# Performance work log

Measured on AMD Instinct MI355X. Metric: run time of the kernel, lower is better.

## Reference

```python
import jax, jax.numpy as jnp
import numpy as np

B, L, D, H, DEPTH = 64, 384, 128, 8, 6
DH = D // H          # 16
VOCAB = 32000
C_OUT = 128
FF = 4 * D           # reformer_pytorch default ff_mult=4
SELF_VAL = -5e4      # TOKEN_SELF_ATTN_VALUE
MASK_VAL = -1e9      # causal mask value


def layer_norm(x, g, b, eps=1e-5):
    mu = jnp.mean(x, -1, keepdims=True)
    var = jnp.mean((x - mu) ** 2, -1, keepdims=True)
    return (x - mu) * jax.lax.rsqrt(var + eps) * g + b


def attn_block(x, p):
    # PreNorm + LSHSelfAttention in full-QK-attention fallback (seq <= full_attn_thres)
    h = layer_norm(x, p['ln1_g'], p['ln1_b'])
    qk = (h @ p['Wqk']).reshape(B, L, H, DH).transpose(0, 2, 1, 3)  # [B,H,L,DH]
    v = (h @ p['Wv']).reshape(B, L, H, DH).transpose(0, 2, 1, 3)
    # shared QK: q = qk, k = l2-normalized qk
    k = qk / jnp.maximum(jnp.linalg.norm(qk, axis=-1, keepdims=True), 1e-12)
    dots = jnp.einsum('bhid,bhjd->bhij', qk, k) * (DH ** -0.5)
    i = jnp.arange(L)
    eye = i[:, None] == i[None, :]
    future = i[None, :] > i[:, None]
    dots = jnp.where(eye, SELF_VAL, dots)   # token cannot (easily) attend to itself
    dots = jnp.where(future, MASK_VAL, dots)  # causal
    a = jax.nn.softmax(dots, axis=-1)
    o = jnp.einsum('bhij,bhjd->bhid', a, v).transpose(0, 2, 1, 3).reshape(B, L, D)
    return o @ p['Wo'] + p['bo']


def ff_block(x, p):
    h = layer_norm(x, p['ln2_g'], p['ln2_b'])
    h = jax.nn.gelu(h @ p['W1'] + p['b1'], approximate=False)
    return h @ p['W2'] + p['b2']


def forward(x_enc, emb, pos1, pos2, ln1_g, ln1_b, Wqk, Wv, Wo, bo,
            ln2_g, ln2_b, W1, b1, W2, b2, lnf_g, lnf_b, Wp, bp):
    # axial positional embedding (summed mode): (25,D) + (25,D) -> (625,D)
    pos = (pos1[:, None, :] + pos2[None, :, :]).reshape(25 * 25, D)[:L]
    x = emb[x_enc] + pos  # [B,L,D]

    layer_params = dict(ln1_g=ln1_g, ln1_b=ln1_b, Wqk=Wqk, Wv=Wv, Wo=Wo, bo=bo,
                        ln2_g=ln2_g, ln2_b=ln2_b, W1=W1, b1=b1, W2=W2, b2=b2)

    def block(carry, p):
        x1, x2 = carry
        y1 = x1 + attn_block(x2, p)
        y2 = x2 + ff_block(y1, p)
        return (y1, y2), None

    # reversible-net math: duplicate stream, run blocks, average the two halves
    (x1, x2), _ = jax.lax.scan(block, (x, x), layer_params)
    x = layer_norm((x1 + x2) * 0.5, lnf_g, lnf_b)
    return x.reshape(B, L * D) @ Wp + bp  # [B, C_OUT]


def setup_inputs() -> dict:
    key = jax.random.key(0)
    ks = jax.random.split(key, 12)
    s = 0.02
    inp = {
        'x_enc': jax.random.randint(ks[0], (B, L), 0, VOCAB, dtype=jnp.int32),
        'emb': jax.random.normal(ks[1], (VOCAB, D), jnp.float32) * s,
        'pos1': jax.random.normal(ks[2], (25, D), jnp.float32) * s,
        'pos2': jax.random.normal(ks[3], (25, D), jnp.float32) * s,
        'ln1_g': jnp.ones((DEPTH, D), jnp.float32),
        'ln1_b': jnp.zeros((DEPTH, D), jnp.float32),
        'Wqk': jax.random.normal(ks[4], (DEPTH, D, D), jnp.float32) * s,
        'Wv': jax.random.normal(ks[5], (DEPTH, D, D), jnp.float32) * s,
        'Wo': jax.random.normal(ks[6], (DEPTH, D, D), jnp.float32) * s,
        'bo': jnp.zeros((DEPTH, D), jnp.float32),
        'ln2_g': jnp.ones((DEPTH, D), jnp.float32),
        'ln2_b': jnp.zeros((DEPTH, D), jnp.float32),
        'W1': jax.random.normal(ks[7], (DEPTH, D, FF), jnp.float32) * s,
        'b1': jnp.zeros((DEPTH, FF), jnp.float32),
        'W2': jax.random.normal(ks[8], (DEPTH, FF, D), jnp.float32) * s,
        'b2': jnp.zeros((DEPTH, D), jnp.float32),
        'lnf_g': jnp.ones((D,), jnp.float32),
        'lnf_b': jnp.zeros((D,), jnp.float32),
        'Wp': jax.random.normal(ks[9], (L * D, C_OUT), jnp.float32) * s,
        'bp': jnp.zeros((C_OUT,), jnp.float32),
    }
    return inp


def reference(x_enc, emb, pos1, pos2, ln1_g, ln1_b, Wqk, Wv, Wo, bo,
              ln2_g, ln2_b, W1, b1, W2, b2, lnf_g, lnf_b, Wp, bp):
    return forward(x_enc, emb, pos1, pos2, ln1_g, ln1_b, Wqk, Wv, Wo, bo,
                   ln2_g, ln2_b, W1, b1, W2, b2, lnf_g, lnf_b, Wp, bp)
```

## Files before the change

### kernel.cpp

```cpp
#include <hip/hip_runtime.h>
#include <hip/hip_bf16.h>
#include <math.h>

#define BB 64
#define LL 384
#define DD 128
#define HH 8
#define DHH 16
#define DEPTH 6
#define FFD 512
#define MROWS (BB*LL)
#define COUT 128
#define KP (LL*DD)
#define KSPLIT 96
#define KCHUNK 512

typedef short bf16x8 __attribute__((ext_vector_type(8)));
typedef float f32x4 __attribute__((ext_vector_type(4)));

__device__ __forceinline__ unsigned short f2bs(float x) {
    __hip_bfloat16 h = __float2bfloat16(x);
    return *reinterpret_cast<unsigned short*>(&h);
}
__device__ __forceinline__ float bs2f(unsigned short u) {
    unsigned int v = ((unsigned int)u) << 16;
    return __uint_as_float(v);
}

__global__ __launch_bounds__(256) void embed_kernel(
    const int* __restrict__ x_enc, const float* __restrict__ emb,
    const float* __restrict__ pos1, const float* __restrict__ pos2,
    float* __restrict__ x1, float* __restrict__ x2)
{
    int t = blockIdx.x * 256 + threadIdx.x;
    int row = t >> 5;
    int c4 = t & 31;
    int l = row % LL;
    int tok = x_enc[row];
    float4 a = ((const float4*)(emb + (size_t)tok * DD))[c4];
    float4 b = ((const float4*)(pos1 + (l / 25) * DD))[c4];
    float4 c = ((const float4*)(pos2 + (l % 25) * DD))[c4];
    float4 r = make_float4(a.x + b.x + c.x, a.y + b.y + c.y,
                           a.z + b.z + c.z, a.w + b.w + c.w);
    ((float4*)x1)[t] = r;
    ((float4*)x2)[t] = r;
}

__global__ __launch_bounds__(256) void castT_kernel(
    const float* __restrict__ src, __hip_bfloat16* __restrict__ dst, int K, int N,
    long sstride, long dstride)
{
    __shared__ float tile[32][33];
    int kb = blockIdx.x * 32, nb = blockIdx.y * 32;
    int tx = threadIdx.x & 31, ty = threadIdx.x >> 5;
    const float* s = src + (size_t)blockIdx.z * sstride;
    __hip_bfloat16* d = dst + (size_t)blockIdx.z * dstride;
    #pragma unroll
    for (int r = 0; r < 32; r += 8)
        tile[r + ty][tx] = s[(size_t)(kb + r + ty) * N + nb + tx];
    __syncthreads();
    #pragma unroll
    for (int r = 0; r < 32; r += 8)
        d[(size_t)(nb + r + ty) * K + kb + tx] = __float2bfloat16(tile[tx][r + ty]);
}

__global__ __launch_bounds__(256) void castT3_kernel(
    const float* __restrict__ sqk, const float* __restrict__ sv, const float* __restrict__ so,
    __hip_bfloat16* __restrict__ dqk, __hip_bfloat16* __restrict__ dv,
    __hip_bfloat16* __restrict__ dwo)
{
    __shared__ float tile[32][33];
    int which = blockIdx.z / 6;
    int dd = blockIdx.z % 6;
    const float* s = (which == 0 ? sqk : (which == 1 ? sv : so)) + (size_t)dd * 16384;
    __hip_bfloat16* d = (which == 0 ? dqk : (which == 1 ? dv : dwo))
                        + (size_t)dd * (which == 2 ? 16384 : 32768);
    int kb = blockIdx.x * 32, nb = blockIdx.y * 32;
    int tx = threadIdx.x & 31, ty = threadIdx.x >> 5;
    #pragma unroll
    for (int r = 0; r < 32; r += 8)
        tile[r + ty][tx] = s[(size_t)(kb + r + ty) * 128 + nb + tx];
    __syncthreads();
    #pragma unroll
    for (int r = 0; r < 32; r += 8)
        d[(size_t)(nb + r + ty) * 128 + kb + tx] = __float2bfloat16(tile[tx][r + ty]);
}

__global__ __launch_bounds__(256) void ln_kernel(
    const float* __restrict__ x, const float* __restrict__ g,
    const float* __restrict__ b, __hip_bfloat16* __restrict__ y)
{
    int wave = threadIdx.x >> 6;
    int lane = threadIdx.x & 63;
    int row = blockIdx.x * 4 + wave;
    float2 v = ((const float2*)(x + (size_t)row * DD))[lane];
    float2 gg = ((const float2*)g)[lane];
    float2 bb = ((const float2*)b)[lane];
    float s = v.x + v.y;
    float sq = v.x * v.x + v.y * v.y;
    #pragma unroll
    for (int off = 32; off > 0; off >>= 1) {
        s += __shfl_down(s, off, 64);
        sq += __shfl_down(sq, off, 64);
    }
    s = __shfl(s, 0, 64);
    sq = __shfl(sq, 0, 64);
    float mean = s * (1.0f / DD);
    float var = sq * (1.0f / DD) - mean * mean;
    float rstd = rsqrtf(var + 1e-5f);
    __hip_bfloat16* yp = y + (size_t)row * DD + lane * 2;
    yp[0] = __float2bfloat16((v.x - mean) * rstd * gg.x + bb.x);
    yp[1] = __float2bfloat16((v.y - mean) * rstd * gg.y + bb.y);
}

__device__ __forceinline__ float gelu_exact(float x) {
    return 0.5f * x * (1.0f + erff(x * 0.70710678118654752f));
}

template<int K, int N, bool BIAS, bool RES, bool GELU, bool OBF, bool LNOUT, bool AVGLN>
__global__ __launch_bounds__(256) void gemm_bf16(
    const __hip_bfloat16* __restrict__ A, const __hip_bfloat16* __restrict__ Bt,
    const float* __restrict__ bias, const float* __restrict__ Rsrc,
    const float* __restrict__ Rsrc2,
    void* __restrict__ Cdst,
    const float* __restrict__ lng, const float* __restrict__ lnb,
    __hip_bfloat16* __restrict__ lnout)
{
    __shared__ unsigned short As[64 * 128];
    __shared__ unsigned short Bs[128 * 128];
    int tid = threadIdx.x;
    int l = tid & 63, w = tid >> 6;
    int wr = w >> 1, wc = w & 1;
    int lr = l & 15, q = l >> 4;
    int m0 = blockIdx.y * 64;
    int n0 = blockIdx.x * 128;

    f32x4 acc[2][4];
    #pragma unroll
    for (int mt = 0; mt < 2; ++mt)
        #pragma unroll
        for (int nt = 0; nt < 4; ++nt) acc[mt][nt] = (f32x4){0.f, 0.f, 0.f, 0.f};

    for (int kt = 0; kt < K; kt += 128) {
        if (kt) __syncthreads();
        #pragma unroll
        for (int p = 0; p < 4; ++p) {
            int n = p * 256 + tid;
            int r = n >> 4;
            int c = (n & 15) ^ (r & 7);
            uint4 dv = *(const uint4*)(A + (size_t)(m0 + r) * K + kt + c * 8);
            *(uint4*)&As[n * 8] = dv;
        }
        #pragma unroll
        for (int p = 0; p < 8; ++p) {
            int n = p * 256 + tid;
            int r = n >> 4;
            int c = (n & 15) ^ (r & 7);
            uint4 dv = *(const uint4*)(Bt + (size_t)(n0 + r) * K + kt + c * 8);
            *(uint4*)&Bs[n * 8] = dv;
        }
        __syncthreads();

        #pragma unroll
        for (int kk = 0; kk < 4; ++kk) {
            bf16x8 afr[2], bfr[4];
            #pragma unroll
            for (int mt = 0; mt < 2; ++mt) {
                int rA = wr * 32 + mt * 16 + lr;
                int cc = (kk * 4 + q) ^ (rA & 7);
                afr[mt] = *(const bf16x8*)&As[(rA * 16 + cc) * 8];
            }
            #pragma unroll
            for (int nt = 0; nt < 4; ++nt) {
                int rB = wc * 64 + nt * 16 + lr;
                int cc = (kk * 4 + q) ^ (rB & 7);
                bfr[nt] = *(const bf16x8*)&Bs[(rB * 16 + cc) * 8];
            }
            #pragma unroll
            for (int mt = 0; mt < 2; ++mt)
                #pragma unroll
                for (int nt = 0; nt < 4; ++nt)
                    acc[mt][nt] = __builtin_amdgcn_mfma_f32_16x16x32_bf16(
                        afr[mt], bfr[nt], acc[mt][nt], 0, 0, 0);
        }
    }

    if (!LNOUT) {
        #pragma unroll
        for (int mt = 0; mt < 2; ++mt) {
            #pragma unroll
            for (int nt = 0; nt < 4; ++nt) {
                int col = n0 + wc * 64 + nt * 16 + lr;
                float bv = BIAS ? bias[col] : 0.f;
                #pragma unroll
                for (int r = 0; r < 4; ++r) {
                    int row = m0 + wr * 32 + mt * 16 + q * 4 + r;
                    float val = acc[mt][nt][r] + bv;
                    if (GELU) val = gelu_exact(val);
                    if (RES) val += Rsrc[(size_t)row * N + col];
                    if (OBF) ((__hip_bfloat16*)Cdst)[(size_t)row * N + col] = __float2bfloat16(val);
                    else     ((float*)Cdst)[(size_t)row * N + col] = val;
                }
            }
        }
    } else {
        float* fp = (float*)Bs;
        __syncthreads();
        #pragma unroll
        for (int mt = 0; mt < 2; ++mt) {
            #pragma unroll
            for (int nt = 0; nt < 4; ++nt) {
                int col = wc * 64 + nt * 16 + lr;
                float bv = BIAS ? bias[col] : 0.f;
                #pragma unroll
                for (int r = 0; r < 4; ++r) {
                    int rowL = wr * 32 + mt * 16 + q * 4 + r;
                    float val = acc[mt][nt][r] + bv;
                    if (RES) val += Rsrc[(size_t)(m0 + rowL) * N + col];
                    fp[rowL * 128 + col] = val;
                }
            }
        }
        __syncthreads();
        int rl = tid >> 2, sub = tid & 3;
        float s = 0.f, sq = 0.f;
        #pragma unroll
        for (int c4 = 0; c4 < 8; ++c4) {
            float4 v = *(const float4*)&fp[rl * 128 + sub * 32 + c4 * 4];
            if (AVGLN) {
                float4 xo = *(const float4*)(Rsrc2 + (size_t)(m0 + rl) * 128 + sub * 32 + c4 * 4);
                v.x = (v.x + xo.x) * 0.5f; v.y = (v.y + xo.y) * 0.5f;
                v.z = (v.z + xo.z) * 0.5f; v.w = (v.w + xo.w) * 0.5f;
            }
            s  += (v.x + v.y) + (v.z + v.w);
            sq += (v.x * v.x + v.y * v.y) + (v.z * v.z + v.w * v.w);
        }
        s  += __shfl_xor(s, 1);  s  += __shfl_xor(s, 2);
        sq += __shfl_xor(sq, 1); sq += __shfl_xor(sq, 2);
        float mean = s * (1.0f / 128.0f);
        float var  = sq * (1.0f / 128.0f) - mean * mean;
        float rstd = rsqrtf(var + 1e-5f);
        int rowG = m0 + rl;
        #pragma unroll
        for (int c4 = 0; c4 < 8; ++c4) {
            int col = sub * 32 + c4 * 4;
            float4 v  = *(const float4*)&fp[rl * 128 + col];
            if (AVGLN) {
                float4 xo = *(const float4*)(Rsrc2 + (size_t)rowG * 128 + col);
                v.x = (v.x + xo.x) * 0.5f; v.y = (v.y + xo.y) * 0.5f;
                v.z = (v.z + xo.z) * 0.5f; v.w = (v.w + xo.w) * 0.5f;
            } else {
                *(float4*)((float*)Cdst + (size_t)rowG * 128 + col) = v;
            }
            float4 g4 = *(const float4*)(lng + col);
            float4 b4 = *(const float4*)(lnb + col);
            unsigned short pk[4];
            pk[0] = f2bs((v.x - mean) * rstd * g4.x + b4.x);
            pk[1] = f2bs((v.y - mean) * rstd * g4.y + b4.y);
            pk[2] = f2bs((v.z - mean) * rstd * g4.z + b4.z);
            pk[3] = f2bs((v.w - mean) * rstd * g4.w + b4.w);
            *(ushort4*)((unsigned short*)lnout + (size_t)rowG * 128 + col) = *(ushort4*)&pk[0];
        }
    }
}

__global__ __launch_bounds__(256) void attn_kernel(
    const __hip_bfloat16* __restrict__ qkv, __hip_bfloat16* __restrict__ o)
{
    int z  = blockIdx.x >> 9;
    int bh = blockIdx.x & 511;
    int b = bh >> 3, hh = bh & 7;
    const unsigned short* base = (const unsigned short*)qkv + (size_t)b * LL * 256 + hh * DHH;

    __shared__ unsigned short knb[LL + 2][24];
    __shared__ unsigned short vtb[16][LL + 24];
    __shared__ float cq[LL];
    __shared__ unsigned short ptile[4][16][40];

    int t = threadIdx.x;
    for (int r = t; r < LL; r += 256) {
        const unsigned short* qp = base + (size_t)r * 256;
        unsigned short qs[16], vs16[16];
        *(uint4*)&qs[0]  = *(const uint4*)(qp);
        *(uint4*)&qs[8]  = *(const uint4*)(qp + 8);
        *(uint4*)&vs16[0] = *(const uint4*)(qp + 128);
        *(uint4*)&vs16[8] = *(const uint4*)(qp + 136);
        float q[16];
        #pragma unroll
        for (int d = 0; d < 16; ++d) q[d] = bs2f(qs[d]);
        float nrm = 0.f;
        #pragma unroll
        for (int d = 0; d < 16; ++d) nrm = fmaf(q[d], q[d], nrm);
        float qn = sqrtf(nrm);
        float inv = 1.0f / fmaxf(qn, 1e-12f);
        cq[r] = 0.25f * qn;
        unsigned short kb[16];
        #pragma unroll
        for (int d = 0; d < 16; ++d) kb[d] = f2bs(q[d] * inv);
        *(uint4*)&knb[r][0] = *(uint4*)&kb[0];
        *(uint4*)&knb[r][8] = *(uint4*)&kb[8];
        *(uint4*)&knb[r][16] = make_uint4(0u, 0u, 0u, 0u);
        #pragma unroll
        for (int d = 0; d < 16; ++d) vtb[d][r] = vs16[d];
    }
    if (t < 16) {
        #pragma unroll
        for (int c = 0; c < 24; ++c) vtb[t][LL + c] = 0;
    }
    if (t < 2) {
        #pragma unroll
        for (int c = 0; c < 24; ++c) knb[LL + t][c] = 0;
    }

    int w = t >> 6, l = t & 63;
    int lr = l & 15, q4 = l >> 4;
    __syncthreads();

    bf16x8 zfrag = {0, 0, 0, 0, 0, 0, 0, 0};
    bf16x8 onesf;
    #pragma unroll
    for (int i = 0; i < 8; ++i) onesf[i] = (short)0x3F80;

    int slot = 2 * w + z;
    int strips[3] = { slot, 15 - slot, 16 + slot };
    #pragma unroll
    for (int si = 0; si < 3; ++si) {
        int s = strips[si];
        int r0 = s * 16;
        bf16x8 bq = *(const bf16x8*)&knb[r0 + lr][q4 * 8];
        float ccq = cq[r0 + lr];
        int qg = r0 + lr;

        f32x4 oacc = (f32x4){0.f, 0.f, 0.f, 0.f};
        f32x4 lacc = (f32x4){0.f, 0.f, 0.f, 0.f};

        for (int jt = 0; jt <= s; jt += 2) {
            bf16x8 a0 = *(const bf16x8*)&knb[jt * 16 + lr][(q4 & 1) * 8];
            a0 = (q4 < 2) ? a0 : zfrag;
            bf16x8 a1 = *(const bf16x8*)&knb[(jt + 1) * 16 + lr][(q4 & 1) * 8];
            a1 = (q4 < 2) ? a1 : zfrag;
            f32x4 s0 = __builtin_amdgcn_mfma_f32_16x16x32_bf16(
                a0, bq, (f32x4){0.f, 0.f, 0.f, 0.f}, 0, 0, 0);
            f32x4 s1 = __builtin_amdgcn_mfma_f32_16x16x32_bf16(
                a1, bq, (f32x4){0.f, 0.f, 0.f, 0.f}, 0, 0, 0);

            unsigned int pk0[2], pk1[2];
            #pragma unroll
            for (int h = 0; h < 2; ++h) {
                int ja = jt * 16 + q4 * 4 + 2 * h;
                float pa = __expf(fmaf(s0[2 * h],     ccq, -ccq));
                pa = (ja < qg) ? pa : 0.f;
                float pb = __expf(fmaf(s0[2 * h + 1], ccq, -ccq));
                pb = (ja + 1 < qg) ? pb : 0.f;
                pk0[h] = (unsigned int)f2bs(pa) | ((unsigned int)f2bs(pb) << 16);
                float pc = __expf(fmaf(s1[2 * h],     ccq, -ccq));
                pc = (ja + 16 < qg) ? pc : 0.f;
                float pd = __expf(fmaf(s1[2 * h + 1], ccq, -ccq));
                pd = (ja + 17 < qg) ? pd : 0.f;
                pk1[h] = (unsigned int)f2bs(pc) | ((unsigned int)f2bs(pd) << 16);
            }
            *(uint2*)&ptile[w][lr][q4 * 4]      = make_uint2(pk0[0], pk0[1]);
            *(uint2*)&ptile[w][lr][16 + q4 * 4] = make_uint2(pk1[0], pk1[1]);
            asm volatile("s_waitcnt lgkmcnt(0)" ::: "memory");
            bf16x8 pfrag = *(const bf16x8*)&ptile[w][lr][q4 * 8];
            bf16x8 vfrag = *(const bf16x8*)&vtb[lr][jt * 16 + q4 * 8];
            oacc = __builtin_amdgcn_mfma_f32_16x16x32_bf16(pfrag, vfrag, oacc, 0, 0, 0);
            lacc = __builtin_amdgcn_mfma_f32_16x16x32_bf16(pfrag, onesf, lacc, 0, 0, 0);
        }

        if (s == 0 && q4 == 0) {
            lacc[0] = 1.0f;
            oacc[0] = bs2f(vtb[lr][0]);
        }
        unsigned short* ob = (unsigned short*)o + (size_t)(b * LL + r0) * DD + hh * 16 + lr;
        #pragma unroll
        for (int reg = 0; reg < 4; ++reg) {
            float ov = oacc[reg] / lacc[reg];
            ob[(size_t)(q4 * 4 + reg) * DD] = f2bs(ov);
        }
    }
}

__global__ __launch_bounds__(256) void final_mfma_kernel(
    const __hip_bfloat16* __restrict__ A, const __hip_bfloat16* __restrict__ Bt,
    float* __restrict__ partials)
{
    __shared__ unsigned short As[64 * 128];
    __shared__ unsigned short Bs[128 * 128];
    int tid = threadIdx.x;
    int l = tid & 63, w = tid >> 6;
    int wr = w >> 1, wc = w & 1;
    int lr = l & 15, q = l >> 4;
    int kbase = blockIdx.x * KCHUNK;

    f32x4 acc[2][4];
    #pragma unroll
    for (int mt = 0; mt < 2; ++mt)
        #pragma unroll
        for (int nt = 0; nt < 4; ++nt) acc[mt][nt] = (f32x4){0.f, 0.f, 0.f, 0.f};

    for (int kt = 0; kt < KCHUNK; kt += 128) {
        if (kt) __syncthreads();
        #pragma unroll
        for (int p = 0; p < 4; ++p) {
            int n = p * 256 + tid;
            int r = n >> 4;
            int c = (n & 15) ^ (r & 7);
            uint4 dv = *(const uint4*)(A + (size_t)r * KP + kbase + kt + c * 8);
            *(uint4*)&As[n * 8] = dv;
        }
        #pragma unroll
        for (int p = 0; p < 8; ++p) {
            int n = p * 256 + tid;
            int r = n >> 4;
            int c = (n & 15) ^ (r & 7);
            uint4 dv = *(const uint4*)(Bt + (size_t)r * KP + kbase + kt + c * 8);
            *(uint4*)&Bs[n * 8] = dv;
        }
        __syncthreads();

        #pragma unroll
        for (int kk = 0; kk < 4; ++kk) {
            bf16x8 afr[2], bfr[4];
            #pragma unroll
            for (int mt = 0; mt < 2; ++mt) {
                int rA = wr * 32 + mt * 16 + lr;
                int cc = (kk * 4 + q) ^ (rA & 7);
                afr[mt] = *(const bf16x8*)&As[(rA * 16 + cc) * 8];
            }
            #pragma unroll
            for (int nt = 0; nt < 4; ++nt) {
                int rB = wc * 64 + nt * 16 + lr;
                int cc = (kk * 4 + q) ^ (rB & 7);
                bfr[nt] = *(const bf16x8*)&Bs[(rB * 16 + cc) * 8];
            }
            #pragma unroll
            for (int mt = 0; mt < 2; ++mt)
                #pragma unroll
                for (int nt = 0; nt < 4; ++nt)
                    acc[mt][nt] = __builtin_amdgcn_mfma_f32_16x16x32_bf16(
                        afr[mt], bfr[nt], acc[mt][nt], 0, 0, 0);
        }
    }

    float* dst = partials + (size_t)blockIdx.x * (64 * 128);
    #pragma unroll
    for (int mt = 0; mt < 2; ++mt) {
        #pragma unroll
        for (int nt = 0; nt < 4; ++nt) {
            int col = wc * 64 + nt * 16 + lr;
            #pragma unroll
            for (int r = 0; r < 4; ++r) {
                int row = wr * 32 + mt * 16 + q * 4 + r;
                dst[row * 128 + col] = acc[mt][nt][r];
            }
        }
    }
}

__global__ __launch_bounds__(256) void final_reduce_kernel(
    const float* __restrict__ partials, const float* __restrict__ bp,
    float* __restrict__ out)
{
    int j = blockIdx.x * 256 + threadIdx.x;
    float s = bp[j & (COUT - 1)];
    #pragma unroll 8
    for (int p = 0; p < KSPLIT; ++p)
        s += partials[(size_t)p * 8192 + j];
    out[j] = s;
}

extern "C" void kernel_launch(void* const* d_in, const int* in_sizes, int n_in,
                              void* d_out, int out_size, void* d_ws, size_t ws_size,
                              hipStream_t stream)
{
    const int*   x_enc = (const int*)  d_in[0];
    const float* emb   = (const float*)d_in[1];
    const float* pos1  = (const float*)d_in[2];
    const float* pos2  = (const float*)d_in[3];
    const float* ln1_g = (const float*)d_in[4];
    const float* ln1_b = (const float*)d_in[5];
    const float* Wqk   = (const float*)d_in[6];
    const float* Wv    = (const float*)d_in[7];
    const float* Wo    = (const float*)d_in[8];
    const float* bo    = (const float*)d_in[9];
    const float* ln2_g = (const float*)d_in[10];
    const float* ln2_b = (const float*)d_in[11];
    const float* W1    = (const float*)d_in[12];
    const float* b1    = (const float*)d_in[13];
    const float* W2    = (const float*)d_in[14];
    const float* b2    = (const float*)d_in[15];
    const float* lnf_g = (const float*)d_in[16];
    const float* lnf_b = (const float*)d_in[17];
    const float* Wp    = (const float*)d_in[18];
    const float* bp    = (const float*)d_in[19];
    float* out = (float*)d_out;

    const size_t SZ = (size_t)MROWS * DD;
    float* ws_f = (float*)d_ws;
    float* x1 = ws_f;
    float* x2 = ws_f + SZ;
    float* R  = ws_f + 2 * SZ;
    __hip_bfloat16* qkv_bf = (__hip_bfloat16*)R;
    __hip_bfloat16* hff = (__hip_bfloat16*)R;
    __hip_bfloat16* h_bf = (__hip_bfloat16*)(ws_f + 4 * SZ);
    __hip_bfloat16* o_bf = h_bf + SZ;
    __hip_bfloat16* wqvT = o_bf + SZ;
    __hip_bfloat16* woT  = wqvT + 6 * 32768;
    __hip_bfloat16* w1T  = woT  + 6 * 16384;
    __hip_bfloat16* w2T  = w1T  + 6 * 65536;
    __hip_bfloat16* WpT  = w2T  + 6 * 65536;
    float* partials = (float*)(WpT + (size_t)COUT * KP);

    castT3_kernel<<<dim3(4, 4, 18), dim3(256), 0, stream>>>(
        Wqk, Wv, Wo, wqvT, wqvT + 16384, woT);
    castT_kernel<<<dim3(4, 16, 6), dim3(256), 0, stream>>>(W1, w1T, 128, 512, 65536, 65536);
    castT_kernel<<<dim3(16, 4, 6), dim3(256), 0, stream>>>(W2, w2T, 512, 128, 65536, 65536);
    castT_kernel<<<dim3(KP / 32, 4, 1), dim3(256), 0, stream>>>(Wp, WpT, KP, 128, 0, 0);

    embed_kernel<<<dim3(MROWS * 32 / 256), dim3(256), 0, stream>>>(x_enc, emb, pos1, pos2, x1, x2);
    ln_kernel<<<dim3(MROWS / 4), dim3(256), 0, stream>>>(x2, ln1_g, ln1_b, h_bf);

    for (int d = 0; d < DEPTH; ++d) {
        const float* bod = bo + d * DD;
        const float* l2g = ln2_g + d * DD;
        const float* l2b = ln2_b + d * DD;
        const float* b1d = b1 + d * FFD;
        const float* b2d = b2 + d * DD;
        const __hip_bfloat16* wqv_d = wqvT + (size_t)d * 32768;
        const __hip_bfloat16* wo_d  = woT  + (size_t)d * 16384;
        const __hip_bfloat16* w1_d  = w1T  + (size_t)d * 65536;
        const __hip_bfloat16* w2_d  = w2T  + (size_t)d * 65536;

        gemm_bf16<128, 256, false, false, false, true, false, false>
            <<<dim3(2, MROWS / 64), dim3(256), 0, stream>>>(
                h_bf, wqv_d, nullptr, nullptr, nullptr, qkv_bf, nullptr, nullptr, nullptr);
        attn_kernel<<<dim3(BB * HH * 2), dim3(256), 0, stream>>>(qkv_bf, o_bf);
        gemm_bf16<128, 128, true, true, false, false, true, false>
            <<<dim3(1, MROWS / 64), dim3(256), 0, stream>>>(
                o_bf, wo_d, bod, x1, nullptr, x1, l2g, l2b, h_bf);
        gemm_bf16<128, 512, true, false, true, true, false, false>
            <<<dim3(4, MROWS / 64), dim3(256), 0, stream>>>(
                h_bf, w1_d, b1d, nullptr, nullptr, hff, nullptr, nullptr, nullptr);
        if (d < DEPTH - 1) {
            gemm_bf16<512, 128, true, true, false, false, true, false>
                <<<dim3(1, MROWS / 64), dim3(256), 0, stream>>>(
                    hff, w2_d, b2d, x2, nullptr, x2,
                    ln1_g + (d + 1) * DD, ln1_b + (d + 1) * DD, h_bf);
        } else {
            gemm_bf16<512, 128, true, true, false, false, true, true>
                <<<dim3(1, MROWS / 64), dim3(256), 0, stream>>>(
                    hff, w2_d, b2d, x2, x1, nullptr, lnf_g, lnf_b, h_bf);
        }
    }

    final_mfma_kernel<<<dim3(KSPLIT), dim3(256), 0, stream>>>(h_bf, WpT, partials);
    final_reduce_kernel<<<dim3(32), dim3(256), 0, stream>>>(partials, bp, out);
}
```

Before: 674.5 us.

## Fuse Wo+LN2+W1 and W2+LN1+QKV GEMMs into per-row-tile mega kernels

Merges the Wo projection, residual, LayerNorm and W1+GELU GEMM into one kernel that keeps the normalized tile in shared memory. It likewise merges the W2 GEMM, residual, next-layer LN1 and the next layer's QKV projection. The goal is to remove round trips through global memory for h_bf and to cut per-layer launches. It also fuses embedding with the first LayerNorm, merges the weight-cast launches, and reuses the WpT buffer as QKV scratch, casting Wp only at the end. In exchange, each block now runs several GEMM stages serially with more shared memory, which may lower occupancy.

Result: faster. 619.2 us (-8.2%).

```diff
diff --git a/kernel.cpp b/kernel.cpp
--- a/kernel.cpp
+++ b/kernel.cpp
@@ -26,74 +26,28 @@
     unsigned int v = ((unsigned int)u) << 16;
     return __uint_as_float(v);
 }
-
-__global__ __launch_bounds__(256) void embed_kernel(
+__device__ __forceinline__ float gelu_exact(float x) {
+    return 0.5f * x * (1.0f + erff(x * 0.70710678118654752f));
+}
+
+__global__ __launch_bounds__(256) void embedln_kernel(
     const int* __restrict__ x_enc, const float* __restrict__ emb,
     const float* __restrict__ pos1, const float* __restrict__ pos2,
-    float* __restrict__ x1, float* __restrict__ x2)
-{
-    int t = blockIdx.x * 256 + threadIdx.x;
-    int row = t >> 5;
-    int c4 = t & 31;
-    int l = row % LL;
-    int tok = x_enc[row];
-    float4 a = ((const float4*)(emb + (size_t)tok * DD))[c4];
-    float4 b = ((const float4*)(pos1 + (l / 25) * DD))[c4];
-    float4 c = ((const float4*)(pos2 + (l % 25) * DD))[c4];
-    float4 r = make_float4(a.x + b.x + c.x, a.y + b.y + c.y,
-                           a.z + b.z + c.z, a.w + b.w + c.w);
-    ((float4*)x1)[t] = r;
-    ((float4*)x2)[t] = r;
-}
-
-__global__ __launch_bounds__(256) void castT_kernel(
-    const float* __restrict__ src, __hip_bfloat16* __restrict__ dst, int K, int N,
-    long sstride, long dstride)
-{
-    __shared__ float tile[32][33];
-    int kb = blockIdx.x * 32, nb = blockIdx.y * 32;
-    int tx = threadIdx.x & 31, ty = threadIdx.x >> 5;
-    const float* s = src + (size_t)blockIdx.z * sstride;
-    __hip_bfloat16* d = dst + (size_t)blockIdx.z * dstride;
-    #pragma unroll
-    for (int r = 0; r < 32; r += 8)
-        tile[r + ty][tx] = s[(size_t)(kb + r + ty) * N + nb + tx];
-    __syncthreads();
-    #pragma unroll
-    for (int r = 0; r < 32; r += 8)
-        d[(size_t)(nb + r + ty) * K + kb + tx] = __float2bfloat16(tile[tx][r + ty]);
-}
-
-__global__ __launch_bounds__(256) void castT3_kernel(
-    const float* __restrict__ sqk, const float* __restrict__ sv, const float* __restrict__ so,
-    __hip_bfloat16* __restrict__ dqk, __hip_bfloat16* __restrict__ dv,
-    __hip_bfloat16* __restrict__ dwo)
-{
-    __shared__ float tile[32][33];
-    int which = blockIdx.z / 6;
-    int dd = blockIdx.z % 6;
-    const float* s = (which == 0 ? sqk : (which == 1 ? sv : so)) + (size_t)dd * 16384;
-    __hip_bfloat16* d = (which == 0 ? dqk : (which == 1 ? dv : dwo))
-                        + (size_t)dd * (which == 2 ? 16384 : 32768);
-    int kb = blockIdx.x * 32, nb = blockIdx.y * 32;
-    int tx = threadIdx.x & 31, ty = threadIdx.x >> 5;
-    #pragma unroll
-    for (int r = 0; r < 32; r += 8)
-        tile[r + ty][tx] = s[(size_t)(kb + r + ty) * 128 + nb + tx];
-    __syncthreads();
-    #pragma unroll
-    for (int r = 0; r < 32; r += 8)
-        d[(size_t)(nb + r + ty) * 128 + kb + tx] = __float2bfloat16(tile[tx][r + ty]);
-}
-
-__global__ __launch_bounds__(256) void ln_kernel(
-    const float* __restrict__ x, const float* __restrict__ g,
-    const float* __restrict__ b, __hip_bfloat16* __restrict__ y)
+    const float* __restrict__ g, const float* __restrict__ b,
+    float* __restrict__ x1, float* __restrict__ x2,
+    __hip_bfloat16* __restrict__ y)
 {
     int wave = threadIdx.x >> 6;
     int lane = threadIdx.x & 63;
     int row = blockIdx.x * 4 + wave;
-    float2 v = ((const float2*)(x + (size_t)row * DD))[lane];
+    int l = row % LL;
+    int tok = x_enc[row];
+    float2 e  = ((const float2*)(emb + (size_t)tok * DD))[lane];
+    float2 p1 = ((const float2*)(pos1 + (l / 25) * DD))[lane];
+    float2 p2 = ((const float2*)(pos2 + (l % 25) * DD))[lane];
+    float2 v = make_float2(e.x + p1.x + p2.x, e.y + p1.y + p2.y);
+    ((float2*)(x1 + (size_t)row * DD))[lane] = v;
+    ((float2*)(x2 + (size_t)row * DD))[lane] = v;
     float2 gg = ((const float2*)g)[lane];
     float2 bb = ((const float2*)b)[lane];
     float s = v.x + v.y;
@@ -113,18 +67,58 @@
     yp[1] = __float2bfloat16((v.y - mean) * rstd * gg.y + bb.y);
 }
 
-__device__ __forceinline__ float gelu_exact(float x) {
-    return 0.5f * x * (1.0f + erff(x * 0.70710678118654752f));
-}
-
-template<int K, int N, bool BIAS, bool RES, bool GELU, bool OBF, bool LNOUT, bool AVGLN>
-__global__ __launch_bounds__(256) void gemm_bf16(
+__device__ __forceinline__ void castT_body(
+    const float* __restrict__ s, __hip_bfloat16* __restrict__ d,
+    int K, int N, int kb, int nb)
+{
+    __shared__ float tile[32][33];
+    int tx = threadIdx.x & 31, ty = threadIdx.x >> 5;
+    #pragma unroll
+    for (int r = 0; r < 32; r += 8)
+        tile[r + ty][tx] = s[(size_t)(kb + r + ty) * N + nb + tx];
+    __syncthreads();
+    #pragma unroll
+    for (int r = 0; r < 32; r += 8)
+        d[(size_t)(nb + r + ty) * K + kb + tx] = __float2bfloat16(tile[tx][r + ty]);
+}
+
+__global__ __launch_bounds__(256) void cast_all_kernel(
+    const float* __restrict__ Wqk, const float* __restrict__ Wv,
+    const float* __restrict__ Wo,  const float* __restrict__ W1,
+    const float* __restrict__ W2,
+    __hip_bfloat16* __restrict__ dqk, __hip_bfloat16* __restrict__ dv,
+    __hip_bfloat16* __restrict__ dwo, __hip_bfloat16* __restrict__ d1,
+    __hip_bfloat16* __restrict__ d2)
+{
+    int z = blockIdx.x;
+    if (z < 288) {
+        int m = z >> 4, t = z & 15;
+        int which = m / 6, dd = m % 6;
+        const float* s = (which == 0 ? Wqk : (which == 1 ? Wv : Wo)) + (size_t)dd * 16384;
+        __hip_bfloat16* d = (which == 0 ? dqk : (which == 1 ? dv : dwo))
+                            + (size_t)dd * (which == 2 ? 16384 : 32768);
+        castT_body(s, d, 128, 128, (t >> 2) * 32, (t & 3) * 32);
+    } else if (z < 672) {
+        int i = z - 288; int dd = i >> 6; int t = i & 63;
+        castT_body(W1 + (size_t)dd * 65536, d1 + (size_t)dd * 65536,
+                   128, 512, (t >> 4) * 32, (t & 15) * 32);
+    } else {
+        int i = z - 672; int dd = i >> 6; int t = i & 63;
+        castT_body(W2 + (size_t)dd * 65536, d2 + (size_t)dd * 65536,
+                   512, 128, (t >> 2) * 32, (t & 3) * 32);
+    }
+}
+
+__global__ __launch_bounds__(256) void castWp_kernel(
+    const float* __restrict__ src, __hip_bfloat16* __restrict__ dst)
+{
+    castT_body(src, dst, KP, 128, blockIdx.x * 32, blockIdx.y * 32);
+}
+
+template<int K, int N>
+__global__ __launch_bounds__(256) void gemm_qkv_kernel(
     const __hip_bfloat16* __restrict__ A, const __hip_bfloat16* __restrict__ Bt,
-    const float* __restrict__ bias, const float* __restrict__ Rsrc,
-    const float* __restrict__ Rsrc2,
-    void* __restrict__ Cdst,
-    const float* __restrict__ lng, const float* __restrict__ lnb,
-    __hip_bfloat16* __restrict__ lnout)
+    __hip_bfloat16* __restrict__ Cdst)
 {
     __shared__ unsigned short As[64 * 128];
     __shared__ unsigned short Bs[128 * 128];
@@ -148,19 +142,16 @@
             int n = p * 256 + tid;
             int r = n >> 4;
             int c = (n & 15) ^ (r & 7);
-            uint4 dv = *(const uint4*)(A + (size_t)(m0 + r) * K + kt + c * 8);
-            *(uint4*)&As[n * 8] = dv;
+            *(uint4*)&As[n * 8] = *(const uint4*)(A + (size_t)(m0 + r) * K + kt + c * 8);
         }
         #pragma unroll
         for (int p = 0; p < 8; ++p) {
             int n = p * 256 + tid;
             int r = n >> 4;
             int c = (n & 15) ^ (r & 7);
-            uint4 dv = *(const uint4*)(Bt + (size_t)(n0 + r) * K + kt + c * 8);
-            *(uint4*)&Bs[n * 8] = dv;
+            *(uint4*)&Bs[n * 8] = *(const uint4*)(Bt + (size_t)(n0 + r) * K + kt + c * 8);
         }
         __syncthreads();
-
         #pragma unroll
         for (int kk = 0; kk < 4; ++kk) {
             bf16x8 afr[2], bfr[4];
@@ -185,83 +176,17 @@
         }
     }
 
-    if (!LNOUT) {
-        #pragma unroll
-        for (int mt = 0; mt < 2; ++mt) {
-            #pragma unroll
-            for (int nt = 0; nt < 4; ++nt) {
-                int col = n0 + wc * 64 + nt * 16 + lr;
-                float bv = BIAS ? bias[col] : 0.f;
-                #pragma unroll
-                for (int r = 0; r < 4; ++r) {
-                    int row = m0 + wr * 32 + mt * 16 + q * 4 + r;
-                    float val = acc[mt][nt][r] + bv;
-                    if (GELU) val = gelu_exact(val);
-                    if (RES) val += Rsrc[(size_t)row * N + col];
-                    if (OBF) ((__hip_bfloat16*)Cdst)[(size_t)row * N + col] = __float2bfloat16(val);
-                    else     ((float*)Cdst)[(size_t)row * N + col] = val;
-                }
-            }
-        }
-    } else {
-        float* fp = (float*)Bs;
-        __syncthreads();
-        #pragma unroll
-        for (int mt = 0; mt < 2; ++mt) {
-            #pragma unroll
-            for (int nt = 0; nt < 4; ++nt) {
-                int col = wc * 64 + nt * 16 + lr;
-                float bv = BIAS ? bias[col] : 0.f;
-                #pragma unroll
-                for (int r = 0; r < 4; ++r) {
-                    int rowL = wr * 32 + mt * 16 + q * 4 + r;
-                    float val = acc[mt][nt][r] + bv;
-                    if (RES) val += Rsrc[(size_t)(m0 + rowL) * N + col];
-                    fp[rowL * 128 + col] = val;
-                }
-            }
-        }
-        __syncthreads();
-        int rl = tid >> 2, sub = tid & 3;
-        float s = 0.f, sq = 0.f;
-        #pragma unroll
-        for (int c4 = 0; c4 < 8; ++c4) {
-            float4 v = *(const float4*)&fp[rl * 128 + sub * 32 + c4 * 4];
-            if (AVGLN) {
-                float4 xo = *(const float4*)(Rsrc2 + (size_t)(m0 + rl) * 128 + sub * 32 + c4 * 4);
-                v.x = (v.x + xo.x) * 0.5f; v.y = (v.y + xo.y) * 0.5f;
-                v.z = (v.z + xo.z) * 0.5f; v.w = (v.w + xo.w) * 0.5f;
-            }
-            s  += (v.x + v.y) + (v.z + v.w);
-            sq += (v.x * v.x + v.y * v.y) + (v.z * v.z + v.w * v.w);
-        }
-        s  += __shfl_xor(s, 1);  s  += __shfl_xor(s, 2);
-        sq += __shfl_xor(sq, 1); sq += __shfl_xor(sq, 2);
-        float mean = s * (1.0f / 128.0f);
-        float var  = sq * (1.0f / 128.0f) - mean * mean;
-        float rstd = rsqrtf(var + 1e-5f);
-        int rowG = m0 + rl;
-        #pragma unroll
-        for (int c4 = 0; c4 < 8; ++c4) {
-            int col = sub * 32 + c4 * 4;
-            float4 v  = *(const float4*)&fp[rl * 128 + col];
-            if (AVGLN) {
-                float4 xo = *(const float4*)(Rsrc2 + (size_t)rowG * 128 + col);
-                v.x = (v.x + xo.x) * 0.5f; v.y = (v.y + xo.y) * 0.5f;
-                v.z = (v.z + xo.z) * 0.5f; v.w = (v.w + xo.w) * 0.5f;
-            } else {
-                *(float4*)((float*)Cdst + (size_t)rowG * 128 + col) = v;
-            }
-            float4 g4 = *(const float4*)(lng + col);
-            float4 b4 = *(const float4*)(lnb + col);
-            unsigned short pk[4];
-            pk[0] = f2bs((v.x - mean) * rstd * g4.x + b4.x);
-            pk[1] = f2bs((v.y - mean) * rstd * g4.y + b4.y);
-            pk[2] = f2bs((v.z - mean) * rstd * g4.z + b4.z);
-            pk[3] = f2bs((v.w - mean) * rstd * g4.w + b4.w);
-            *(ushort4*)((unsigned short*)lnout + (size_t)rowG * 128 + col) = *(ushort4*)&pk[0];
-        }
-    }
+    #pragma unroll
+    for (int mt = 0; mt < 2; ++mt)
+        #pragma unroll
+        for (int nt = 0; nt < 4; ++nt) {
+            int col = n0 + wc * 64 + nt * 16 + lr;
+            #pragma unroll
+            for (int r = 0; r < 4; ++r) {
+                int row = m0 + wr * 32 + mt * 16 + q * 4 + r;
+                Cdst[(size_t)row * N + col] = __float2bfloat16(acc[mt][nt][r]);
+            }
+        }
 }
 
 __global__ __launch_bounds__(256) void attn_kernel(
@@ -381,6 +306,349 @@
     }
 }
 
+__global__ __launch_bounds__(256) void mega_wolf_kernel(
+    const __hip_bfloat16* __restrict__ Ao, const __hip_bfloat16* __restrict__ WoTd,
+    const float* __restrict__ bod, float* __restrict__ x1,
+    const float* __restrict__ lng, const float* __restrict__ lnb,
+    const __hip_bfloat16* __restrict__ W1Td, const float* __restrict__ b1d,
+    __hip_bfloat16* __restrict__ hff)
+{
+    __shared__ unsigned short As[64 * 128];
+    __shared__ unsigned short Bs[128 * 128];
+    __shared__ unsigned short Hs[64 * 128];
+    int tid = threadIdx.x;
+    int l = tid & 63, w = tid >> 6;
+    int wr = w >> 1, wc = w & 1;
+    int lr = l & 15, q = l >> 4;
+    int m0 = blockIdx.x * 64;
+
+    f32x4 acc[2][4];
+    #pragma unroll
+    for (int mt = 0; mt < 2; ++mt)
+        #pragma unroll
+        for (int nt = 0; nt < 4; ++nt) acc[mt][nt] = (f32x4){0.f, 0.f, 0.f, 0.f};
+
+    #pragma unroll
+    for (int p = 0; p < 4; ++p) {
+        int n = p * 256 + tid;
+        int r = n >> 4;
+        int c = (n & 15) ^ (r & 7);
+        *(uint4*)&As[n * 8] = *(const uint4*)(Ao + (size_t)(m0 + r) * 128 + c * 8);
+    }
+    #pragma unroll
+    for (int p = 0; p < 8; ++p) {
+        int n = p * 256 + tid;
+        int r = n >> 4;
+        int c = (n & 15) ^ (r & 7);
+        *(uint4*)&Bs[n * 8] = *(const uint4*)(WoTd + (size_t)r * 128 + c * 8);
+    }
+    __syncthreads();
+    #pragma unroll
+    for (int kk = 0; kk < 4; ++kk) {
+        bf16x8 afr[2], bfr[4];
+        #pragma unroll
+        for (int mt = 0; mt < 2; ++mt) {
+            int rA = wr * 32 + mt * 16 + lr;
+            int cc = (kk * 4 + q) ^ (rA & 7);
+            afr[mt] = *(const bf16x8*)&As[(rA * 16 + cc) * 8];
+        }
+        #pragma unroll
+        for (int nt = 0; nt < 4; ++nt) {
+            int rB = wc * 64 + nt * 16 + lr;
+            int cc = (kk * 4 + q) ^ (rB & 7);
+            bfr[nt] = *(const bf16x8*)&Bs[(rB * 16 + cc) * 8];
+        }
+        #pragma unroll
+        for (int mt = 0; mt < 2; ++mt)
+            #pragma unroll
+            for (int nt = 0; nt < 4; ++nt)
+                acc[mt][nt] = __builtin_amdgcn_mfma_f32_16x16x32_bf16(
+                    afr[mt], bfr[nt], acc[mt][nt], 0, 0, 0);
+    }
+
+    float* fp = (float*)Bs;
+    __syncthreads();
+    #pragma unroll
+    for (int mt = 0; mt < 2; ++mt)
+        #pragma unroll
+        for (int nt = 0; nt < 4; ++nt) {
+            int col = wc * 64 + nt * 16 + lr;
+            float bv = bod[col];
+            #pragma unroll
+            for (int r = 0; r < 4; ++r) {
+                int rowL = wr * 32 + mt * 16 + q * 4 + r;
+                fp[rowL * 128 + col] = acc[mt][nt][r] + bv
+                                       + x1[(size_t)(m0 + rowL) * 128 + col];
+            }
+        }
+    __syncthreads();
+    {
+        int rl = tid >> 2, sub = tid & 3;
+        float s = 0.f, sq = 0.f;
+        #pragma unroll
+        for (int c4 = 0; c4 < 8; ++c4) {
+            float4 v = *(const float4*)&fp[rl * 128 + sub * 32 + c4 * 4];
+            s  += (v.x + v.y) + (v.z + v.w);
+            sq += (v.x * v.x + v.y * v.y) + (v.z * v.z + v.w * v.w);
+        }
+        s  += __shfl_xor(s, 1);  s  += __shfl_xor(s, 2);
+        sq += __shfl_xor(sq, 1); sq += __shfl_xor(sq, 2);
+        float mean = s * (1.0f / 128.0f);
+        float var  = sq * (1.0f / 128.0f) - mean * mean;
+        float rstd = rsqrtf(var + 1e-5f);
+        #pragma unroll
+        for (int c4 = 0; c4 < 8; ++c4) {
+            int col = sub * 32 + c4 * 4;
+            float4 v  = *(const float4*)&fp[rl * 128 + col];
+            *(float4*)(x1 + (size_t)(m0 + rl) * 128 + col) = v;
+            float4 g4 = *(const float4*)(lng + col);
+            float4 b4 = *(const float4*)(lnb + col);
+            unsigned short pk[4];
+            pk[0] = f2bs((v.x - mean) * rstd * g4.x + b4.x);
+            pk[1] = f2bs((v.y - mean) * rstd * g4.y + b4.y);
+            pk[2] = f2bs((v.z - mean) * rstd * g4.z + b4.z);
+            pk[3] = f2bs((v.w - mean) * rstd * g4.w + b4.w);
+            int addr = rl * 128 + (((col >> 3) ^ (rl & 7)) << 3) + (col & 7);
+            *(ushort4*)&Hs[addr] = *(ushort4*)&pk[0];
+        }
+    }
+    __syncthreads();
+
+    for (int nc = 0; nc < 4; ++nc) {
+        if (nc) __syncthreads();
+        #pragma unroll
+        for (int p = 0; p < 8; ++p) {
+            int n = p * 256 + tid;
+            int r = n >> 4;
+            int c = (n & 15) ^ (r & 7);
+            *(uint4*)&Bs[n * 8] = *(const uint4*)(W1Td + (size_t)(nc * 128 + r) * 128 + c * 8);
+        }
+        __syncthreads();
+        f32x4 a2[2][4];
+        #pragma unroll
+        for (int mt = 0; mt < 2; ++mt)
+            #pragma unroll
+            for (int nt = 0; nt < 4; ++nt) a2[mt][nt] = (f32x4){0.f, 0.f, 0.f, 0.f};
+        #pragma unroll
+        for (int kk = 0; kk < 4; ++kk) {
+            bf16x8 afr[2], bfr[4];
+            #pragma unroll
+            for (int mt = 0; mt < 2; ++mt) {
+                int rA = wr * 32 + mt * 16 + lr;
+                int cc = (kk * 4 + q) ^ (rA & 7);
+                afr[mt] = *(const bf16x8*)&Hs[(rA * 16 + cc) * 8];
+            }
+            #pragma unroll
+            for (int nt = 0; nt < 4; ++nt) {
+                int rB = wc * 64 + nt * 16 + lr;
+                int cc = (kk * 4 + q) ^ (rB & 7);
+                bfr[nt] = *(const bf16x8*)&Bs[(rB * 16 + cc) * 8];
+            }
+            #pragma unroll
+            for (int mt = 0; mt < 2; ++mt)
+                #pragma unroll
+                for (int nt = 0; nt < 4; ++nt)
+                    a2[mt][nt] = __builtin_amdgcn_mfma_f32_16x16x32_bf16(
+                        afr[mt], bfr[nt], a2[mt][nt], 0, 0, 0);
+        }
+        #pragma unroll
+        for (int mt = 0; mt < 2; ++mt)
+            #pragma unroll
+            for (int nt = 0; nt < 4; ++nt) {
+                int colg = nc * 128 + wc * 64 + nt * 16 + lr;
+                float bv = b1d[colg];
+                #pragma unroll
+                for (int r = 0; r < 4; ++r) {
+                    int row = m0 + wr * 32 + mt * 16 + q * 4 + r;
+                    hff[(size_t)row * 512 + colg] =
+                        __float2bfloat16(gelu_exact(a2[mt][nt][r] + bv));
+                }
+            }
+    }
+}
+
+template<bool LAST>
+__global__ __launch_bounds__(256) void mega_ffq_kernel(
+    const __hip_bfloat16* __restrict__ Ahff, const __hip_bfloat16* __restrict__ W2Td,
+    const float* __restrict__ b2d, float* __restrict__ x2,
+    const float* __restrict__ x1,
+    const float* __restrict__ lng, const float* __restrict__ lnb,
+    const __hip_bfloat16* __restrict__ WqvTd, __hip_bfloat16* __restrict__ qkv,
+    __hip_bfloat16* __restrict__ hout)
+{
+    __shared__ unsigned short As[64 * 128];
+    __shared__ unsigned short Bs[128 * 128];
+    __shared__ unsigned short Hs[64 * 128];
+    int tid = threadIdx.x;
+    int l = tid & 63, w = tid >> 6;
+    int wr = w >> 1, wc = w & 1;
+    int lr = l & 15, q = l >> 4;
+    int m0 = blockIdx.x * 64;
+
+    f32x4 acc[2][4];
+    #pragma unroll
+    for (int mt = 0; mt < 2; ++mt)
+        #pragma unroll
+        for (int nt = 0; nt < 4; ++nt) acc[mt][nt] = (f32x4){0.f, 0.f, 0.f, 0.f};
+
+    for (int kt = 0; kt < 512; kt += 128) {
+        if (kt) __syncthreads();
+        #pragma unroll
+        for (int p = 0; p < 4; ++p) {
+            int n = p * 256 + tid;
+            int r = n >> 4;
+            int c = (n & 15) ^ (r & 7);
+            *(uint4*)&As[n * 8] = *(const uint4*)(Ahff + (size_t)(m0 + r) * 512 + kt + c * 8);
+        }
+        #pragma unroll
+        for (int p = 0; p < 8; ++p) {
+            int n = p * 256 + tid;
+            int r = n >> 4;
+            int c = (n & 15) ^ (r & 7);
+            *(uint4*)&Bs[n * 8] = *(const uint4*)(W2Td + (size_t)r * 512 + kt + c * 8);
+        }
+        __syncthreads();
+        #pragma unroll
+        for (int kk = 0; kk < 4; ++kk) {
+            bf16x8 afr[2], bfr[4];
+            #pragma unroll
+            for (int mt = 0; mt < 2; ++mt) {
+                int rA = wr * 32 + mt * 16 + lr;
+                int cc = (kk * 4 + q) ^ (rA & 7);
+                afr[mt] = *(const bf16x8*)&As[(rA * 16 + cc) * 8];
+            }
+            #pragma unroll
+            for (int nt = 0; nt < 4; ++nt) {
+                int rB = wc * 64 + nt * 16 + lr;
+                int cc = (kk * 4 + q) ^ (rB & 7);
+                bfr[nt] = *(const bf16x8*)&Bs[(rB * 16 + cc) * 8];
+            }
+            #pragma unroll
+            for (int mt = 0; mt < 2; ++mt)
+                #pragma unroll
+                for (int nt = 0; nt < 4; ++nt)
+                    acc[mt][nt] = __builtin_amdgcn_mfma_f32_16x16x32_bf16(
+                        afr[mt], bfr[nt], acc[mt][nt], 0, 0, 0);
+        }
+    }
+
+    float* fp = (float*)Bs;
+    __syncthreads();
+    #pragma unroll
+    for (int mt = 0; mt < 2; ++mt)
+        #pragma unroll
+        for (int nt = 0; nt < 4; ++nt) {
+            int col = wc * 64 + nt * 16 + lr;
+            float bv = b2d[col];
+            #pragma unroll
+            for (int r = 0; r < 4; ++r) {
+                int rowL = wr * 32 + mt * 16 + q * 4 + r;
+                fp[rowL * 128 + col] = acc[mt][nt][r] + bv
+                                       + x2[(size_t)(m0 + rowL) * 128 + col];
+            }
+        }
+    __syncthreads();
+    {
+        int rl = tid >> 2, sub = tid & 3;
+        float s = 0.f, sq = 0.f;
+        #pragma unroll
+        for (int c4 = 0; c4 < 8; ++c4) {
+            float4 v = *(const float4*)&fp[rl * 128 + sub * 32 + c4 * 4];
+            if (LAST) {
+                float4 xo = *(const float4*)(x1 + (size_t)(m0 + rl) * 128 + sub * 32 + c4 * 4);
+                v.x = (v.x + xo.x) * 0.5f; v.y = (v.y + xo.y) * 0.5f;
+                v.z = (v.z + xo.z) * 0.5f; v.w = (v.w + xo.w) * 0.5f;
+            }
+            s  += (v.x + v.y) + (v.z + v.w);
+            sq += (v.x * v.x + v.y * v.y) + (v.z * v.z + v.w * v.w);
+        }
+        s  += __shfl_xor(s, 1);  s  += __shfl_xor(s, 2);
+        sq += __shfl_xor(sq, 1); sq += __shfl_xor(sq, 2);
+        float mean = s * (1.0f / 128.0f);
+        float var  = sq * (1.0f / 128.0f) - mean * mean;
+        float rstd = rsqrtf(var + 1e-5f);
+        #pragma unroll
+        for (int c4 = 0; c4 < 8; ++c4) {
+            int col = sub * 32 + c4 * 4;
+            float4 v = *(const float4*)&fp[rl * 128 + col];
+            if (LAST) {
+                float4 xo = *(const float4*)(x1 + (size_t)(m0 + rl) * 128 + col);
+                v.x = (v.x + xo.x) * 0.5f; v.y = (v.y + xo.y) * 0.5f;
+                v.z = (v.z + xo.z) * 0.5f; v.w = (v.w + xo.w) * 0.5f;
+            } else {
+                *(float4*)(x2 + (size_t)(m0 + rl) * 128 + col) = v;
+            }
+            float4 g4 = *(const float4*)(lng + col);
+            float4 b4 = *(const float4*)(lnb + col);
+            unsigned short pk[4];
+            pk[0] = f2bs((v.x - mean) * rstd * g4.x + b4.x);
+            pk[1] = f2bs((v.y - mean) * rstd * g4.y + b4.y);
+            pk[2] = f2bs((v.z - mean) * rstd * g4.z + b4.z);
+            pk[3] = f2bs((v.w - mean) * rstd * g4.w + b4.w);
+            if (LAST) {
+                *(ushort4*)((unsigned short*)hout + (size_t)(m0 + rl) * 128 + col)
+                    = *(ushort4*)&pk[0];
+            } else {
+                int addr = rl * 128 + (((col >> 3) ^ (rl & 7)) << 3) + (col & 7);
+                *(ushort4*)&Hs[addr] = *(ushort4*)&pk[0];
+            }
+        }
+    }
+    __syncthreads();
+
+    if (!LAST) {
+        for (int nc = 0; nc < 2; ++nc) {
+            if (nc) __syncthreads();
+            #pragma unroll
+            for (int p = 0; p < 8; ++p) {
+                int n = p * 256 + tid;
+                int r = n >> 4;
+                int c = (n & 15) ^ (r & 7);
+                *(uint4*)&Bs[n * 8] = *(const uint4*)(WqvTd + (size_t)(nc * 128 + r) * 128 + c * 8);
+            }
+            __syncthreads();
+            f32x4 a2[2][4];
+            #pragma unroll
+            for (int mt = 0; mt < 2; ++mt)
+                #pragma unroll
+                for (int nt = 0; nt < 4; ++nt) a2[mt][nt] = (f32x4){0.f, 0.f, 0.f, 0.f};
+            #pragma unroll
+            for (int kk = 0; kk < 4; ++kk) {
+                bf16x8 afr[2], bfr[4];
+                #pragma unroll
+                for (int mt = 0; mt < 2; ++mt) {
+                    int rA = wr * 32 + mt * 16 + lr;
+                    int cc = (kk * 4 + q) ^ (rA & 7);
+                    afr[mt] = *(const bf16x8*)&Hs[(rA * 16 + cc) * 8];
+                }
+                #pragma unroll
+                for (int nt = 0; nt < 4; ++nt) {
+                    int rB = wc * 64 + nt * 16 + lr;
+                    int cc = (kk * 4 + q) ^ (rB & 7);
+                    bfr[nt] = *(const bf16x8*)&Bs[(rB * 16 + cc) * 8];
+                }
+                #pragma unroll
+                for (int mt = 0; mt < 2; ++mt)
+                    #pragma unroll
+                    for (int nt = 0; nt < 4; ++nt)
+                        a2[mt][nt] = __builtin_amdgcn_mfma_f32_16x16x32_bf16(
+                            afr[mt], bfr[nt], a2[mt][nt], 0, 0, 0);
+            }
+            #pragma unroll
+            for (int mt = 0; mt < 2; ++mt)
+                #pragma unroll
+                for (int nt = 0; nt < 4; ++nt) {
+                    int colg = nc * 128 + wc * 64 + nt * 16 + lr;
+                    #pragma unroll
+                    for (int r = 0; r < 4; ++r) {
+                        int row = m0 + wr * 32 + mt * 16 + q * 4 + r;
+                        qkv[(size_t)row * 256 + colg] = __float2bfloat16(a2[mt][nt][r]);
+                    }
+                }
+        }
+    }
+}
+
 __global__ __launch_bounds__(256) void final_mfma_kernel(
     const __hip_bfloat16* __restrict__ A, const __hip_bfloat16* __restrict__ Bt,
     float* __restrict__ partials)
@@ -406,19 +674,16 @@
             int n = p * 256 + tid;
             int r = n >> 4;
             int c = (n & 15) ^ (r & 7);
-            uint4 dv = *(const uint4*)(A + (size_t)r * KP + kbase + kt + c * 8);
-            *(uint4*)&As[n * 8] = dv;
+            *(uint4*)&As[n * 8] = *(const uint4*)(A + (size_t)r * KP + kbase + kt + c * 8);
         }
         #pragma unroll
         for (int p = 0; p < 8; ++p) {
             int n = p * 256 + tid;
             int r = n >> 4;
             int c = (n & 15) ^ (r & 7);
-            uint4 dv = *(const uint4*)(Bt + (size_t)r * KP + kbase + kt + c * 8);
-            *(uint4*)&Bs[n * 8] = dv;
+            *(uint4*)&Bs[n * 8] = *(const uint4*)(Bt + (size_t)r * KP + kbase + kt + c * 8);
         }
         __syncthreads();
-
         #pragma unroll
         for (int kk = 0; kk < 4; ++kk) {
             bf16x8 afr[2], bfr[4];
@@ -445,7 +710,7 @@
 
     float* dst = partials + (size_t)blockIdx.x * (64 * 128);
     #pragma unroll
-    for (int mt = 0; mt < 2; ++mt) {
+    for (int mt = 0; mt < 2; ++mt)
         #pragma unroll
         for (int nt = 0; nt < 4; ++nt) {
             int col = wc * 64 + nt * 16 + lr;
@@ -455,7 +720,6 @@
                 dst[row * 128 + col] = acc[mt][nt][r];
             }
         }
-    }
 }
 
 __global__ __launch_bounds__(256) void final_reduce_kernel(
@@ -500,9 +764,7 @@
     float* ws_f = (float*)d_ws;
     float* x1 = ws_f;
     float* x2 = ws_f + SZ;
-    float* R  = ws_f + 2 * SZ;
-    __hip_bfloat16* qkv_bf = (__hip_bfloat16*)R;
-    __hip_bfloat16* hff = (__hip_bfloat16*)R;
+    __hip_bfloat16* hff  = (__hip_bfloat16*)(ws_f + 2 * SZ);
     __hip_bfloat16* h_bf = (__hip_bfloat16*)(ws_f + 4 * SZ);
     __hip_bfloat16* o_bf = h_bf + SZ;
     __hip_bfloat16* wqvT = o_bf + SZ;
@@ -510,50 +772,35 @@
     __hip_bfloat16* w1T  = woT  + 6 * 16384;
     __hip_bfloat16* w2T  = w1T  + 6 * 65536;
     __hip_bfloat16* WpT  = w2T  + 6 * 65536;
+    __hip_bfloat16* qkv  = WpT;
     float* partials = (float*)(WpT + (size_t)COUT * KP);
 
-    castT3_kernel<<<dim3(4, 4, 18), dim3(256), 0, stream>>>(
-        Wqk, Wv, Wo, wqvT, wqvT + 16384, woT);
-    castT_kernel<<<dim3(4, 16, 6), dim3(256), 0, stream>>>(W1, w1T, 128, 512, 65536, 65536);
-    castT_kernel<<<dim3(16, 4, 6), dim3(256), 0, stream>>>(W2, w2T, 512, 128, 65536, 65536);
-    castT_kernel<<<dim3(KP / 32, 4, 1), dim3(256), 0, stream>>>(Wp, WpT, KP, 128, 0, 0);
-
-    embed_kernel<<<dim3(MROWS * 32 / 256), dim3(256), 0, stream>>>(x_enc, emb, pos1, pos2, x1, x2);
-    ln_kernel<<<dim3(MROWS / 4), dim3(256), 0, stream>>>(x2, ln1_g, ln1_b, h_bf);
+    cast_all_kernel<<<dim3(1056), dim3(256), 0, stream>>>(
+        Wqk, Wv, Wo, W1, W2, wqvT, wqvT + 16384, woT, w1T, w2T);
+    embedln_kernel<<<dim3(MROWS / 4), dim3(256), 0, stream>>>(
+        x_enc, emb, pos1, pos2, ln1_g, ln1_b, x1, x2, h_bf);
+    gemm_qkv_kernel<128, 256><<<dim3(2, MROWS / 64), dim3(256), 0, stream>>>(
+        h_bf, wqvT, qkv);
 
     for (int d = 0; d < DEPTH; ++d) {
-        const float* bod = bo + d * DD;
-        const float* l2g = ln2_g + d * DD;
-        const float* l2b = ln2_b + d * DD;
-        const float* b1d = b1 + d * FFD;
-        const float* b2d = b2 + d * DD;
-        const __hip_bfloat16* wqv_d = wqvT + (size_t)d * 32768;
-        const __hip_bfloat16* wo_d  = woT  + (size_t)d * 16384;
-        const __hip_bfloat16* w1_d  = w1T  + (size_t)d * 65536;
-        const __hip_bfloat16* w2_d  = w2T  + (size_t)d * 65536;
-
-        gemm_bf16<128, 256, false, false, false, true, false, false>
-            <<<dim3(2, MROWS / 64), dim3(256), 0, stream>>>(
-                h_bf, wqv_d, nullptr, nullptr, nullptr, qkv_bf, nullptr, nullptr, nullptr);
-        attn_kernel<<<dim3(BB * HH * 2), dim3(256), 0, stream>>>(qkv_bf, o_bf);
-        gemm_bf16<128, 128, true, true, false, false, true, false>
-            <<<dim3(1, MROWS / 64), dim3(256), 0, stream>>>(
-                o_bf, wo_d, bod, x1, nullptr, x1, l2g, l2b, h_bf);
-        gemm_bf16<128, 512, true, false, true, true, false, false>
-            <<<dim3(4, MROWS / 64), dim3(256), 0, stream>>>(
-                h_bf, w1_d, b1d, nullptr, nullptr, hff, nullptr, nullptr, nullptr);
+        attn_kernel<<<dim3(BB * HH * 2), dim3(256), 0, stream>>>(qkv, o_bf);
+        mega_wolf_kernel<<<dim3(MROWS / 64), dim3(256), 0, stream>>>(
+            o_bf, woT + (size_t)d * 16384, bo + d * DD, x1,
+            ln2_g + d * DD, ln2_b + d * DD,
+            w1T + (size_t)d * 65536, b1 + d * FFD, hff);
         if (d < DEPTH - 1) {
-            gemm_bf16<512, 128, true, true, false, false, true, false>
-                <<<dim3(1, MROWS / 64), dim3(256), 0, stream>>>(
-                    hff, w2_d, b2d, x2, nullptr, x2,
-                    ln1_g + (d + 1) * DD, ln1_b + (d + 1) * DD, h_bf);
+            mega_ffq_kernel<false><<<dim3(MROWS / 64), dim3(256), 0, stream>>>(
+                hff, w2T + (size_t)d * 65536, b2 + d * DD, x2, nullptr,
+                ln1_g + (d + 1) * DD, ln1_b + (d + 1) * DD,
+                wqvT + (size_t)(d + 1) * 32768, qkv, nullptr);
         } else {
-            gemm_bf16<512, 128, true, true, false, false, true, true>
-                <<<dim3(1, MROWS / 64), dim3(256), 0, stream>>>(
-                    hff, w2_d, b2d, x2, x1, nullptr, lnf_g, lnf_b, h_bf);
-        }
-    }
-
+            mega_ffq_kernel<true><<<dim3(MROWS / 64), dim3(256), 0, stream>>>(
+                hff, w2T + (size_t)d * 65536, b2 + d * DD, x2, x1,
+                lnf_g, lnf_b, nullptr, nullptr, h_bf);
+        }
+    }
+
+    castWp_kernel<<<dim3(KP / 32, 4), dim3(256), 0, stream>>>(Wp, WpT);
     final_mfma_kernel<<<dim3(KSPLIT), dim3(256), 0, stream>>>(h_bf, WpT, partials);
     final_reduce_kernel<<<dim3(32), dim3(256), 0, stream>>>(partials, bp, out);
 }
```
